# Kernel tuning notes

Measured on AMD Instinct MI355X. Metric: run time of the kernel, lower is better.

## Reference

```python
import jax, jax.numpy as jnp
import numpy as np

NUM_GROUPS = 32
EPS = 1e-6


def group_norm(x, gamma, beta):
    # x: (B, C, H, W)
    B, C, H, W = x.shape
    g = x.reshape(B, NUM_GROUPS, C // NUM_GROUPS, H, W)
    mean = g.mean(axis=(2, 3, 4), keepdims=True)
    var = g.var(axis=(2, 3, 4), keepdims=True)
    g = (g - mean) / jnp.sqrt(var + EPS)
    g = g.reshape(B, C, H, W)
    return g * gamma[None, :, None, None] + beta[None, :, None, None]


def nin(x, W, b):
    # 1x1 linear projection over channel dim
    return jnp.einsum('bchw,cd->bdhw', x, W) + b[None, :, None, None]


def setup_inputs() -> dict:
    key = jax.random.key(0)
    ks = jax.random.split(key, 8)
    B, C, H, W = 32, 512, 32, 32
    lim = np.sqrt(3 * 0.1 / C)  # NIN init_scale=0.1 uniform limit
    return {
        'x': jax.random.normal(ks[0], (B, C, H, W), jnp.float32),
        'gamma': jnp.ones((C,), jnp.float32),
        'beta': jnp.zeros((C,), jnp.float32),
        'Wq': jax.random.uniform(ks[1], (C, C), jnp.float32, -lim, lim),
        'bq': jnp.zeros((C,), jnp.float32),
        'Wk': jax.random.uniform(ks[2], (C, C), jnp.float32, -lim, lim),
        'bk': jnp.zeros((C,), jnp.float32),
        'Wv': jax.random.uniform(ks[3], (C, C), jnp.float32, -lim, lim),
        'bv': jnp.zeros((C,), jnp.float32),
        'Wp': jax.random.normal(ks[4], (C, C), jnp.float32) * 1e-5,  # init_scale=0.0 -> ~0
        'bp': jnp.zeros((C,), jnp.float32),
    }


def reference(x, gamma, beta, Wq, bq, Wk, bk, Wv, bv, Wp, bp):
    B, C, H, W = x.shape
    h = group_norm(x, gamma, beta)
    q = nin(h, Wq, bq)
    k = nin(h, Wk, bk)
    v = nin(h, Wv, bv)
    # full (HW)x(HW) attention weights, as the original materializes
    w = jnp.einsum('bchw,bcHW->bhwHW', q, k) * (C ** -0.5)
    w = w.reshape(B, H, W, H * W)
    w = jax.nn.softmax(w, axis=-1)
    w = w.reshape(B, H, W, H, W)
    h_out = jnp.einsum('bhwHW,bcHW->bchw', w, v)
    h_out = nin(h_out, Wp, bp)
    return x + h_out
```

## Files before the change

kernel.cpp:

```cpp
#include <hip/hip_runtime.h>
#include <hip/hip_bf16.h>
#include <math.h>

typedef __attribute__((ext_vector_type(8))) short bf16x8;
typedef __attribute__((ext_vector_type(4))) float f32x4;

typedef const __attribute__((address_space(1))) unsigned int guint;
typedef __attribute__((address_space(3))) unsigned int luint;

static __device__ __forceinline__ short f2bf(float f) {
    union { float f; unsigned u; } a; a.f = f;
    unsigned r = 0x7FFFu + ((a.u >> 16) & 1u);
    return (short)((a.u + r) >> 16);
}
static __device__ __forceinline__ float bf2f(short s) {
    union { unsigned u; float f; } a;
    a.u = ((unsigned)(unsigned short)s) << 16;
    return a.f;
}

__global__ __launch_bounds__(256)
void transpose_w(const float* __restrict__ w0, const float* __restrict__ w1,
                 const float* __restrict__ w2, const float* __restrict__ w3,
                 short* __restrict__ outT, float qscale)
{
    __shared__ float ld[32][33];
    const float* W = (blockIdx.z == 0) ? w0 : (blockIdx.z == 1) ? w1
                   : (blockIdx.z == 2) ? w2 : w3;
    const float sc = (blockIdx.z == 0) ? qscale : 1.f;
    short* O = outT + (long long)blockIdx.z * 512 * 512;
    const int tx = threadIdx.x & 31, ty = threadIdx.x >> 5;
    const int c0 = blockIdx.y * 32, d0 = blockIdx.x * 32;
#pragma unroll
    for (int r = 0; r < 4; ++r)
        ld[ty + 8 * r][tx] = W[(long long)(c0 + ty + 8 * r) * 512 + d0 + tx];
    __syncthreads();
#pragma unroll
    for (int r = 0; r < 4; ++r)
        O[(long long)(d0 + ty + 8 * r) * 512 + c0 + tx] = f2bf(ld[tx][ty + 8 * r] * sc);
}

__global__ __launch_bounds__(256)
void concat_bias(const float* __restrict__ bq, const float* __restrict__ bk,
                 float* __restrict__ bqk, float qscale)
{
    int i = blockIdx.x * 256 + threadIdx.x;
    bqk[i] = (i < 512) ? bq[i] * qscale : bk[i - 512];
}

__global__ __launch_bounds__(256)
void gn_stats(const float* __restrict__ x, float2* __restrict__ stats)
{
    const int bg = blockIdx.x;
    const float4* p = reinterpret_cast<const float4*>(x + (long long)bg * 16384);
    float s = 0.f, ss = 0.f;
    for (int i = threadIdx.x; i < 4096; i += 256) {
        float4 v = p[i];
        s  += v.x + v.y + v.z + v.w;
        ss += v.x * v.x + v.y * v.y + v.z * v.z + v.w * v.w;
    }
    __shared__ float rs[256], rss[256];
    rs[threadIdx.x] = s; rss[threadIdx.x] = ss;
    __syncthreads();
    for (int o = 128; o > 0; o >>= 1) {
        if (threadIdx.x < o) { rs[threadIdx.x] += rs[threadIdx.x + o];
                               rss[threadIdx.x] += rss[threadIdx.x + o]; }
        __syncthreads();
    }
    if (threadIdx.x == 0) {
        float mean = rs[0] * (1.f / 16384.f);
        float var  = rss[0] * (1.f / 16384.f) - mean * mean;
        stats[bg] = make_float2(mean, rsqrtf(var + 1e-6f));
    }
}

__global__ __launch_bounds__(256)
void gn_apply_t(const float* __restrict__ x, const float2* __restrict__ stats,
                const float* __restrict__ gamma, const float* __restrict__ beta,
                short* __restrict__ hn)
{
    __shared__ short lds[32 * 520];
    const int t = threadIdx.x;
    const int s0 = blockIdx.x * 32;
    const int b  = blockIdx.y;
#pragma unroll
    for (int i = 0; i < 16; ++i) {
        int qi = t + 256 * i;
        int c = qi >> 3, sc = qi & 7;
        float4 v = *reinterpret_cast<const float4*>(
            x + ((long long)(b * 512 + c)) * 1024 + s0 + sc * 4);
        float2 st = stats[b * 32 + (c >> 4)];
        float ga = gamma[c], be = beta[c];
        float m = st.x, r = st.y;
        lds[(sc * 4 + 0) * 520 + c] = f2bf((v.x - m) * r * ga + be);
        lds[(sc * 4 + 1) * 520 + c] = f2bf((v.y - m) * r * ga + be);
        lds[(sc * 4 + 2) * 520 + c] = f2bf((v.z - m) * r * ga + be);
        lds[(sc * 4 + 3) * 520 + c] = f2bf((v.w - m) * r * ga + be);
    }
    __syncthreads();
#pragma unroll
    for (int i = 0; i < 8; ++i) {
        int p = t + 256 * i;
        int s = p >> 6, j = p & 63;
        float4 v = *reinterpret_cast<const float4*>(&lds[s * 520 + j * 8]);
        *reinterpret_cast<float4*>(
            hn + ((long long)(b * 1024 + s0 + s)) * 512 + j * 8) = v;
    }
}

template<int BIAS_M, int BIAS_N, int RESID, int EXPOUT, int DIVROW>
__global__ __launch_bounds__(512, 2)
void nt_gemm(const short* __restrict__ A, const short* __restrict__ B,
             void* __restrict__ Cv,
             const float* __restrict__ biasM, const float* __restrict__ biasN,
             const float* __restrict__ resid, const float* __restrict__ rs,
             int rsM, float scale, int K, int lda, int ldb, int ldc,
             long long sA, long long sB, long long sC,
             int tilesM, int tilesPerBatch)
{
    __shared__ short lsA[2][2][128 * 64];
    __shared__ short lsB[2][2][128 * 64];

    const int id = blockIdx.x;
    const int chunk = gridDim.x >> 3;
    const int gid = (id & 7) * chunk + (id >> 3);
    const int bz = gid / tilesPerBatch;
    const int tt = gid - bz * tilesPerBatch;
    const int m0 = (tt % tilesM) * 256;
    const int n0 = (tt / tilesM) * 256;

    const int t = threadIdx.x;
    const int lane = t & 63;
    const int w = t >> 6;
    const int wrs = w >> 1;
    const int wcs = w & 1;
    const int lr16 = lane & 15, lkg = lane >> 4;
    const int sw = lr16 & 7;

    const int srow = t >> 3;
    const int scol = ((t & 7) ^ (srow & 7)) * 8;
    const short* gA = A + (long long)bz * sA + (long long)(m0 + srow) * lda + scol;
    const short* gB = B + (long long)bz * sB + (long long)(n0 + srow) * ldb + scol;

    f32x4 acc[4][2][4];
#pragma unroll
    for (int q = 0; q < 4; ++q)
#pragma unroll
        for (int i = 0; i < 2; ++i)
#pragma unroll
            for (int j = 0; j < 4; ++j) acc[q][i][j] = (f32x4){0.f, 0.f, 0.f, 0.f};

    const int nk = K >> 6;

#define STAGE_A(buf, h, kt)                                                    \
    {                                                                          \
        _Pragma("unroll")                                                      \
        for (int c = 0; c < 2; ++c)                                            \
            __builtin_amdgcn_global_load_lds(                                  \
                (guint*)(gA + (long long)((h) * 128 + 64 * c) * lda + (kt) * 64), \
                (luint*)&lsA[buf][h][t * 8 + 4096 * c], 16, 0, 0);             \
    }
#define STAGE_B(buf, h, kt)                                                    \
    {                                                                          \
        _Pragma("unroll")                                                      \
        for (int c = 0; c < 2; ++c)                                            \
            __builtin_amdgcn_global_load_lds(                                  \
                (guint*)(gB + (long long)((h) * 128 + 64 * c) * ldb + (kt) * 64), \
                (luint*)&lsB[buf][h][t * 8 + 4096 * c], 16, 0, 0);             \
    }

#define LDA_HALF(dst, buf, h)                                                  \
    _Pragma("unroll")                                                          \
    for (int mi2 = 0; mi2 < 2; ++mi2)                                          \
        _Pragma("unroll")                                                      \
        for (int ks = 0; ks < 2; ++ks)                                         \
            dst[mi2][ks] = *reinterpret_cast<const bf16x8*>(                   \
                &lsA[buf][h][(wrs * 32 + mi2 * 16 + lr16) * 64 +               \
                             (((ks * 4 + lkg) ^ sw) * 8)]);
#define LDB_HALF(dst, buf, h)                                                  \
    _Pragma("unroll")                                                          \
    for (int ni = 0; ni < 4; ++ni)                                             \
        _Pragma("unroll")                                                      \
        for (int ks = 0; ks < 2; ++ks)                                         \
            dst[ni][ks] = *reinterpret_cast<const bf16x8*>(                    \
                &lsB[buf][h][(wcs * 64 + ni * 16 + lr16) * 64 +                \
                             (((ks * 4 + lkg) ^ sw) * 8)]);

#define LGKM0                                                                  \
    asm volatile("s_waitcnt lgkmcnt(0)" ::: "memory");                         \
    __builtin_amdgcn_sched_barrier(0)

#define MFMAQ(q, Af, Bf)                                                       \
    _Pragma("unroll")                                                          \
    for (int ks = 0; ks < 2; ++ks)                                             \
        _Pragma("unroll")                                                      \
        for (int mi2 = 0; mi2 < 2; ++mi2)                                      \
            _Pragma("unroll")                                                  \
            for (int ni = 0; ni < 4; ++ni)                                     \
                acc[q][mi2][ni] = __builtin_amdgcn_mfma_f32_16x16x32_bf16(     \
                    Af[mi2][ks], Bf[ni][ks], acc[q][mi2][ni], 0, 0, 0);

#define FRAME(b, kt)                                                           \
    {                                                                          \
        bf16x8 a0[2][2], a1[2][2], b0f[4][2], b1f[4][2];                       \
                                \
        LDB_HALF(b0f, b, 0)                                                    \
        LDA_HALF(a0, b, 0)                                                     \
        STAGE_B((b) ^ 1, 0, (kt) + 1);                                         \
        STAGE_B((b) ^ 1, 1, (kt) + 1);                                         \
        STAGE_A((b) ^ 1, 0, (kt) + 1);                                         \
        LGKM0;                                                                 \
        LDB_HALF(b1f, b, 1)                                                    \
        __builtin_amdgcn_s_setprio(1);                                         \
        MFMAQ(0, a0, b0f)                                                      \
        __builtin_amdgcn_s_setprio(0);                                         \
        LGKM0;                                                                 \
        __builtin_amdgcn_s_setprio(1);                                         \
        MFMAQ(1, a0, b1f)                                                      \
        __builtin_amdgcn_s_setprio(0);                                         \
        __builtin_amdgcn_sched_barrier(0);                                     \
        asm volatile("s_waitcnt vmcnt(6)" ::: "memory");                       \
        __builtin_amdgcn_s_barrier();                                          \
              \
        LDA_HALF(a1, b, 1)                                                     \
        STAGE_A((b) ^ 1, 1, (kt) + 1);                                         \
        LGKM0;                                                                 \
        __builtin_amdgcn_s_setprio(1);                                         \
        MFMAQ(2, a1, b0f)                                                      \
        MFMAQ(3, a1, b1f)                                                      \
        __builtin_amdgcn_s_setprio(0);                                         \
        __builtin_amdgcn_sched_barrier(0);                                     \
        asm volatile("s_waitcnt vmcnt(2)" ::: "memory");                       \
        __builtin_amdgcn_s_barrier();                                          \
    }

    STAGE_B(0, 0, 0); STAGE_B(0, 1, 0); STAGE_A(0, 0, 0);
    STAGE_A(0, 1, 0);
    asm volatile("s_waitcnt vmcnt(2)" ::: "memory");
    __builtin_amdgcn_sched_barrier(0);
    __builtin_amdgcn_s_barrier();

    for (int kt = 0; kt < nk; kt += 2) {
        FRAME(0, kt)
        FRAME(1, kt + 1)
    }
#undef STAGE_A
#undef STAGE_B
#undef LDA_HALF
#undef LDB_HALF
#undef LGKM0
#undef MFMAQ
#undef FRAME

#pragma unroll
    for (int ah = 0; ah < 2; ++ah) {
#pragma unroll
        for (int bh = 0; bh < 2; ++bh) {
#pragma unroll
            for (int mi2 = 0; mi2 < 2; ++mi2) {
                float addm[4], mul[4];
#pragma unroll
                for (int j = 0; j < 4; ++j) {
                    const int rrow = m0 + ah * 128 + wrs * 32 + mi2 * 16 + lkg * 4 + j;
                    addm[j] = BIAS_M ? biasM[rrow] : 0.f;
                    mul[j]  = DIVROW ? 1.f / rs[(long long)bz * rsM + rrow] : 1.f;
                }
#pragma unroll
                for (int ni = 0; ni < 4; ++ni) {
                    const int col = n0 + bh * 128 + wcs * 64 + ni * 16 + lr16;
                    float bn = BIAS_N ? biasN[col] : 0.f;
#pragma unroll
                    for (int j = 0; j < 4; ++j) {
                        const int rrow = m0 + ah * 128 + wrs * 32 + mi2 * 16 + lkg * 4 + j;
                        float v2 = acc[ah * 2 + bh][mi2][ni][j] + addm[j] + bn;
                        v2 *= scale;
                        if (EXPOUT) v2 = __expf(v2 - 8.f);
                        if (DIVROW) v2 *= mul[j];
                        const long long idx = (long long)rrow * ldc + col;
                        if (RESID) {
                            float* Cf = (float*)Cv + (long long)bz * sC;
                            Cf[idx] = v2 + resid[(long long)bz * sC + idx];
                        } else {
                            short* Cs = (short*)Cv + (long long)bz * sC;
                            Cs[idx] = f2bf(v2);
                        }
                    }
                }
            }
        }
    }
}

__global__ __launch_bounds__(256)
void rowsum_rows(const short* __restrict__ S, float* __restrict__ rs)
{
    const int wave = threadIdx.x >> 6, lane = threadIdx.x & 63;
    const long long row = (long long)blockIdx.x * 4 + wave;
    const short* p = S + row * 1024;
    bf16x8 h0 = *reinterpret_cast<const bf16x8*>(p + lane * 8);
    bf16x8 h1 = *reinterpret_cast<const bf16x8*>(p + 512 + lane * 8);
    float s = 0.f;
#pragma unroll
    for (int j = 0; j < 8; ++j) s += bf2f(h0[j]) + bf2f(h1[j]);
#pragma unroll
    for (int o = 32; o > 0; o >>= 1) s += __shfl_xor(s, o);
    if (lane == 0) rs[row] = s;
}

extern "C" void kernel_launch(void* const* d_in, const int* in_sizes, int n_in,
                              void* d_out, int out_size, void* d_ws, size_t ws_size,
                              hipStream_t stream)
{
    (void)in_sizes; (void)n_in; (void)out_size; (void)ws_size;
    const float* x     = (const float*)d_in[0];
    const float* gamma = (const float*)d_in[1];
    const float* beta  = (const float*)d_in[2];
    const float* Wq = (const float*)d_in[3];
    const float* bq = (const float*)d_in[4];
    const float* Wk = (const float*)d_in[5];
    const float* bk = (const float*)d_in[6];
    const float* Wv = (const float*)d_in[7];
    const float* bv = (const float*)d_in[8];
    const float* Wp = (const float*)d_in[9];
    const float* bp = (const float*)d_in[10];
    float* out = (float*)d_out;

    char* ws = (char*)d_ws;
    short*  expS = (short*)ws;
    short*  hn   = (short*)ws;
    short*  qkb  = (short*)(ws + (64LL << 20));
    short*  vbuf = (short*)(ws + (128LL << 20));
    short*  wT   = (short*)(ws + (160LL << 20));
    float2* stats = (float2*)(ws + (162LL << 20));
    float*  bqk   = (float*)(ws + (162LL << 20) + (16 << 10));
    float*  rs    = (float*)(ws + (162LL << 20) + (32 << 10));
    short*  ho    = qkb;

    const short* WqkT = wT;
    const short* WvT  = wT + 2 * 512 * 512;
    const short* WpT  = wT + 3 * 512 * 512;

    const float qscale = 0.044194173824159216f;

    transpose_w<<<dim3(16, 16, 4), 256, 0, stream>>>(Wq, Wk, Wv, Wp, wT, qscale);
    concat_bias<<<dim3(4), 256, 0, stream>>>(bq, bk, bqk, qscale);
    gn_stats<<<dim3(1024), 256, 0, stream>>>(x, stats);
    gn_apply_t<<<dim3(32, 32), 256, 0, stream>>>(x, stats, gamma, beta, hn);

    nt_gemm<0, 1, 0, 0, 0><<<512, 512, 0, stream>>>(
        hn, WqkT, qkb, nullptr, bqk, nullptr, nullptr, 0, 1.f,
        512, 512, 512, 1024, 1024 * 512, 0, 1024LL * 1024, 4, 16);
    nt_gemm<1, 0, 0, 0, 0><<<256, 512, 0, stream>>>(
        WvT, hn, vbuf, bv, nullptr, nullptr, nullptr, 0, 1.f,
        512, 512, 512, 1024, 0, 1024 * 512, 512 * 1024, 2, 8);
    nt_gemm<0, 0, 0, 1, 0><<<512, 512, 0, stream>>>(
        qkb, qkb + 512, expS, nullptr, nullptr, nullptr, nullptr, 0, 1.f,
        512, 1024, 1024, 1024, 1024LL * 1024, 1024LL * 1024, 1024LL * 1024, 4, 16);
    rowsum_rows<<<dim3(8192), 256, 0, stream>>>(expS, rs);
    nt_gemm<0, 0, 0, 0, 1><<<256, 512, 0, stream>>>(
        expS, vbuf, ho, nullptr, nullptr, nullptr, rs, 1024, 1.f,
        1024, 1024, 1024, 512, 1024LL * 1024, 512 * 1024, 1024 * 512, 4, 8);
    nt_gemm<1, 0, 1, 0, 0><<<256, 512, 0, stream>>>(
        WpT, ho, out, bp, nullptr, x, nullptr, 0, 1.f,
        512, 512, 512, 1024, 0, 1024 * 512, 512LL * 1024, 2, 8);
}
```

Before: 231.2 us.

## Fuse softmax row-sum into exp GEMM epilogue and drop rowsum kernel

The QK^T GEMM epilogue now accumulates per-row partial sums of the exponentiated scores, reduces them with lane shuffles and shared memory, and writes four partial sums per row (one per 256-column tile). The PV GEMM adds the four partials before taking the reciprocal. This removes a separate kernel launch and a full re-read of the bf16 score matrix. Launch bounds also drop from 2 to 1 blocks per CU, which frees registers for the extra accumulators but may reduce occupancy. Row sums now come from the fp32 values before bf16 rounding, so they differ slightly from sums of the stored scores.

```diff
diff --git a/kernel.cpp b/kernel.cpp
--- a/kernel.cpp
+++ b/kernel.cpp
@@ -108,13 +108,13 @@
     }
 }
 
-template<int BIAS_M, int BIAS_N, int RESID, int EXPOUT, int DIVROW>
-__global__ __launch_bounds__(512, 2)
+template<int BIAS_M, int BIAS_N, int RESID, int EXPRS, int DIVROW4>
+__global__ __launch_bounds__(512, 1)
 void nt_gemm(const short* __restrict__ A, const short* __restrict__ B,
              void* __restrict__ Cv,
              const float* __restrict__ biasM, const float* __restrict__ biasN,
-             const float* __restrict__ resid, const float* __restrict__ rs,
-             int rsM, float scale, int K, int lda, int ldb, int ldc,
+             const float* __restrict__ resid, float* __restrict__ rs,
+             float scale, int K, int lda, int ldb, int ldc,
              long long sA, long long sB, long long sC,
              int tilesM, int tilesPerBatch)
 {
@@ -252,6 +252,15 @@
 #undef MFMAQ
 #undef FRAME
 
+    float psum[2][2][4];
+    if (EXPRS) {
+#pragma unroll
+        for (int ah = 0; ah < 2; ++ah)
+#pragma unroll
+            for (int mi2 = 0; mi2 < 2; ++mi2)
+#pragma unroll
+                for (int j = 0; j < 4; ++j) psum[ah][mi2][j] = 0.f;
+    }
 #pragma unroll
     for (int ah = 0; ah < 2; ++ah) {
 #pragma unroll
@@ -263,7 +272,10 @@
                 for (int j = 0; j < 4; ++j) {
                     const int rrow = m0 + ah * 128 + wrs * 32 + mi2 * 16 + lkg * 4 + j;
                     addm[j] = BIAS_M ? biasM[rrow] : 0.f;
-                    mul[j]  = DIVROW ? 1.f / rs[(long long)bz * rsM + rrow] : 1.f;
+                    if (DIVROW4) {
+                        const float* r4 = rs + (long long)bz * 4096 + rrow;
+                        mul[j] = 1.f / (r4[0] + r4[1024] + r4[2048] + r4[3072]);
+                    } else mul[j] = 1.f;
                 }
 #pragma unroll
                 for (int ni = 0; ni < 4; ++ni) {
@@ -274,8 +286,8 @@
                         const int rrow = m0 + ah * 128 + wrs * 32 + mi2 * 16 + lkg * 4 + j;
                         float v2 = acc[ah * 2 + bh][mi2][ni][j] + addm[j] + bn;
                         v2 *= scale;
-                        if (EXPOUT) v2 = __expf(v2 - 8.f);
-                        if (DIVROW) v2 *= mul[j];
+                        if (EXPRS) { v2 = __expf(v2 - 8.f); psum[ah][mi2][j] += v2; }
+                        if (DIVROW4) v2 *= mul[j];
                         const long long idx = (long long)rrow * ldc + col;
                         if (RESID) {
                             float* Cf = (float*)Cv + (long long)bz * sC;
@@ -289,22 +301,34 @@
             }
         }
     }
-}
-
-__global__ __launch_bounds__(256)
-void rowsum_rows(const short* __restrict__ S, float* __restrict__ rs)
-{
-    const int wave = threadIdx.x >> 6, lane = threadIdx.x & 63;
-    const long long row = (long long)blockIdx.x * 4 + wave;
-    const short* p = S + row * 1024;
-    bf16x8 h0 = *reinterpret_cast<const bf16x8*>(p + lane * 8);
-    bf16x8 h1 = *reinterpret_cast<const bf16x8*>(p + 512 + lane * 8);
-    float s = 0.f;
-#pragma unroll
-    for (int j = 0; j < 8; ++j) s += bf2f(h0[j]) + bf2f(h1[j]);
-#pragma unroll
-    for (int o = 32; o > 0; o >>= 1) s += __shfl_xor(s, o);
-    if (lane == 0) rs[row] = s;
+    if (EXPRS) {
+#pragma unroll
+        for (int ah = 0; ah < 2; ++ah)
+#pragma unroll
+            for (int mi2 = 0; mi2 < 2; ++mi2)
+#pragma unroll
+                for (int j = 0; j < 4; ++j) {
+                    float v = psum[ah][mi2][j];
+                    v += __shfl_xor(v, 1); v += __shfl_xor(v, 2);
+                    v += __shfl_xor(v, 4); v += __shfl_xor(v, 8);
+                    psum[ah][mi2][j] = v;
+                }
+        float* scr = (float*)&lsA[1][0][0];
+        if (lr16 == 0) {
+#pragma unroll
+            for (int ah = 0; ah < 2; ++ah)
+#pragma unroll
+                for (int mi2 = 0; mi2 < 2; ++mi2)
+#pragma unroll
+                    for (int j = 0; j < 4; ++j)
+                        scr[wcs * 256 + ah * 128 + wrs * 32 + mi2 * 16 + lkg * 4 + j]
+                            = psum[ah][mi2][j];
+        }
+        __syncthreads();
+        if (t < 256)
+            rs[(long long)bz * 4096 + (n0 >> 8) * 1024 + m0 + t]
+                = scr[t] + scr[256 + t];
+    }
 }
 
 extern "C" void kernel_launch(void* const* d_in, const int* in_sizes, int n_in,
@@ -333,7 +357,7 @@
     short*  wT   = (short*)(ws + (160LL << 20));
     float2* stats = (float2*)(ws + (162LL << 20));
     float*  bqk   = (float*)(ws + (162LL << 20) + (16 << 10));
-    float*  rs    = (float*)(ws + (162LL << 20) + (32 << 10));
+    float*  rs4   = (float*)(ws + (162LL << 20) + (32 << 10));
     short*  ho    = qkb;
 
     const short* WqkT = wT;
@@ -348,19 +372,18 @@
     gn_apply_t<<<dim3(32, 32), 256, 0, stream>>>(x, stats, gamma, beta, hn);
 
     nt_gemm<0, 1, 0, 0, 0><<<512, 512, 0, stream>>>(
-        hn, WqkT, qkb, nullptr, bqk, nullptr, nullptr, 0, 1.f,
+        hn, WqkT, qkb, nullptr, bqk, nullptr, nullptr, 1.f,
         512, 512, 512, 1024, 1024 * 512, 0, 1024LL * 1024, 4, 16);
     nt_gemm<1, 0, 0, 0, 0><<<256, 512, 0, stream>>>(
-        WvT, hn, vbuf, bv, nullptr, nullptr, nullptr, 0, 1.f,
+        WvT, hn, vbuf, bv, nullptr, nullptr, nullptr, 1.f,
         512, 512, 512, 1024, 0, 1024 * 512, 512 * 1024, 2, 8);
     nt_gemm<0, 0, 0, 1, 0><<<512, 512, 0, stream>>>(
-        qkb, qkb + 512, expS, nullptr, nullptr, nullptr, nullptr, 0, 1.f,
+        qkb, qkb + 512, expS, nullptr, nullptr, nullptr, rs4, 1.f,
         512, 1024, 1024, 1024, 1024LL * 1024, 1024LL * 1024, 1024LL * 1024, 4, 16);
-    rowsum_rows<<<dim3(8192), 256, 0, stream>>>(expS, rs);
     nt_gemm<0, 0, 0, 0, 1><<<256, 512, 0, stream>>>(
-        expS, vbuf, ho, nullptr, nullptr, nullptr, rs, 1024, 1.f,
+        expS, vbuf, ho, nullptr, nullptr, nullptr, rs4, 1.f,
         1024, 1024, 1024, 512, 1024LL * 1024, 512 * 1024, 1024 * 512, 4, 8);
     nt_gemm<1, 0, 1, 0, 0><<<256, 512, 0, stream>>>(
-        WpT, ho, out, bp, nullptr, x, nullptr, 0, 1.f,
+        WpT, ho, out, bp, nullptr, x, nullptr, 1.f,
         512, 512, 512, 1024, 0, 1024 * 512, 512LL * 1024, 2, 8);
 }
```

Measured after the change: 224.2 us. -3.0%, faster.
